# Optimization experiments

Measured on AMD Instinct MI355X. Metric: run time of the kernel, lower is better.

Reference implementation:

```python
import jax, jax.numpy as jnp
import numpy as np

V = 50000

def _spmm(edge_vals, edge_row, edge_col, x):
    # sparse (V,V) @ dense (V,F) via gather + segment_sum
    return jax.ops.segment_sum(edge_vals[:, None] * x[edge_col], edge_row, num_segments=V)

def setup_inputs() -> dict:
    key = jax.random.key(0)
    ks = jax.random.split(key, 6)
    B, Cin, Cout, K, E = 4, 128, 128, 4, 800000
    x = jax.random.normal(ks[0], (B, Cin, V), dtype=jnp.float32)
    edge_row = jax.random.randint(ks[1], (E,), 0, V, dtype=jnp.int32)
    edge_col = jax.random.randint(ks[2], (E,), 0, V, dtype=jnp.int32)
    edge_vals = jax.random.normal(ks[3], (E,), dtype=jnp.float32) * 0.05
    std = np.sqrt(2.0 / (Cin * K)).astype(np.float32)
    weights = jax.random.normal(ks[4], (K, Cin, Cout), dtype=jnp.float32) * std
    biases = jnp.full((Cout,), 0.01, dtype=jnp.float32)
    return {"x": x, "edge_row": edge_row, "edge_col": edge_col,
            "edge_vals": edge_vals, "weights": weights, "biases": biases}

def reference(x, edge_row, edge_col, edge_vals, weights, biases):
    B, Cin, Vv = x.shape
    K = weights.shape[0]
    # (B,Cin,V) -> (V, B*Cin)
    x0 = jnp.transpose(x, (2, 0, 1)).reshape(Vv, B * Cin)
    xs = [x0]
    if K > 1:
        x1 = _spmm(edge_vals, edge_row, edge_col, x0)
        xs.append(x1)
        for _ in range(2, K):
            x2 = 2.0 * _spmm(edge_vals, edge_row, edge_col, x1) - x0
            xs.append(x2)
            x0, x1 = x1, x2
    xk = jnp.stack(xs, 0).reshape(K, Vv, B, Cin)
    # tensordot over (K, Cin): (K,V,B,Cin) x (K,Cin,Cout) -> (V,B,Cout)
    out = jnp.einsum('kvbc,kco->vbo', xk, weights)
    out = out + biases
    # permute (V,B,Cout) -> (B,Cout,V)
    return jnp.transpose(out, (1, 2, 0))
```

## Files before the change

kernel.cpp:

```cpp
#include <hip/hip_runtime.h>

#define V_N   50000
#define B_N   4
#define C_IN  128
#define C_OUT 128
#define E_N   800000
#define F_N   512
#define M_TOT 200000

#define SCAN_BLK  1024
#define SCAN_NB   ((V_N + SCAN_BLK - 1) / SCAN_BLK)

typedef unsigned short ushort_t;
typedef __attribute__((ext_vector_type(8))) short short8;
typedef __attribute__((ext_vector_type(4))) float f32x4;

__device__ __forceinline__ float bf_lo(unsigned u) { return __uint_as_float(u << 16); }
__device__ __forceinline__ float bf_hi(unsigned u) { return __uint_as_float(u & 0xFFFF0000u); }
__device__ __forceinline__ ushort_t f2bf(float f) {
    unsigned u = __float_as_uint(f);
    u += 0x7FFFu + ((u >> 16) & 1u);
    return (ushort_t)(u >> 16);
}

__global__ __launch_bounds__(256) void k_transpose_in(const float* __restrict__ x,
                                                      ushort_t* __restrict__ x0) {
    __shared__ float tile[32][33];
    int vb = blockIdx.x * 32;
    int fb = blockIdx.y * 32;
    int tx = threadIdx.x, ty = threadIdx.y;
#pragma unroll
    for (int i = 0; i < 32; i += 8) {
        int f = fb + ty + i, v = vb + tx;
        float val = 0.f;
        if (v < V_N) val = x[(size_t)f * V_N + v];
        tile[ty + i][tx] = val;
    }
    __syncthreads();
#pragma unroll
    for (int i = 0; i < 32; i += 8) {
        int v = vb + ty + i, f = fb + tx;
        if (v < V_N) x0[(size_t)v * F_N + f] = f2bf(tile[tx][ty + i]);
    }
}

__global__ __launch_bounds__(256) void k_hist(const int* __restrict__ row,
                                              int* __restrict__ counts) {
    int e = blockIdx.x * blockDim.x + threadIdx.x;
    if (e < E_N) atomicAdd(&counts[row[e]], 1);
}

__global__ __launch_bounds__(256) void k_scan_blk(const int* __restrict__ counts,
                                                  int* __restrict__ row_ptr,
                                                  int* __restrict__ blk_sums) {
    __shared__ int s[256];
    int t = threadIdx.x;
    int base = blockIdx.x * SCAN_BLK + t * 4;
    int c0 = (base + 0 < V_N) ? counts[base + 0] : 0;
    int c1 = (base + 1 < V_N) ? counts[base + 1] : 0;
    int c2 = (base + 2 < V_N) ? counts[base + 2] : 0;
    int c3 = (base + 3 < V_N) ? counts[base + 3] : 0;
    int p1 = c0, p2 = c0 + c1, p3 = c0 + c1 + c2, tot = p3 + c3;
    s[t] = tot;
    __syncthreads();
#pragma unroll
    for (int off = 1; off < 256; off <<= 1) {
        int v = (t >= off) ? s[t - off] : 0;
        __syncthreads();
        s[t] += v;
        __syncthreads();
    }
    int excl = (t == 0) ? 0 : s[t - 1];
    if (base + 0 < V_N) row_ptr[base + 0] = excl;
    if (base + 1 < V_N) row_ptr[base + 1] = excl + p1;
    if (base + 2 < V_N) row_ptr[base + 2] = excl + p2;
    if (base + 3 < V_N) row_ptr[base + 3] = excl + p3;
    if (t == 255) blk_sums[blockIdx.x] = s[255];
}

__global__ __launch_bounds__(64) void k_scan_top(const int* __restrict__ blk_sums,
                                                 int* __restrict__ blk_off) {
    int t = threadIdx.x;
    int v = (t < SCAN_NB) ? blk_sums[t] : 0;
#pragma unroll
    for (int off = 1; off < 64; off <<= 1) {
        int u = __shfl_up(v, off);
        if (t >= off) v += u;
    }
    blk_off[t] = v;
}

__global__ __launch_bounds__(256) void k_scan_add(const int* __restrict__ blk_off,
                                                  int* __restrict__ row_ptr,
                                                  int* __restrict__ next) {
    int b = blockIdx.x, t = threadIdx.x;
    int off = (b == 0) ? 0 : blk_off[b - 1];
    int base = b * SCAN_BLK + t * 4;
#pragma unroll
    for (int i = 0; i < 4; i++) {
        int idx = base + i;
        if (idx < V_N) {
            int rv = row_ptr[idx] + off;
            row_ptr[idx] = rv;
            next[idx]    = rv;
        }
    }
    if (b == 0 && t == 0) row_ptr[V_N] = blk_off[SCAN_NB - 1];
}

__global__ __launch_bounds__(256) void k_scatter(const int* __restrict__ row,
                                                 const int* __restrict__ col,
                                                 const float* __restrict__ vals,
                                                 int* __restrict__ next,
                                                 int2* __restrict__ edges) {
    int e = blockIdx.x * blockDim.x + threadIdx.x;
    if (e < E_N) {
        int r = row[e];
        int pos = atomicAdd(&next[r], 1);
        edges[pos] = make_int2(col[e], __float_as_int(vals[e]));
    }
}

__global__ __launch_bounds__(256) void k_wprep(const float* __restrict__ W,
                                               ushort_t* __restrict__ Wt) {
    int i = blockIdx.x * 256 + threadIdx.x;
    int k = i >> 14, c = (i >> 7) & 127, o = i & 127;
    Wt[((size_t)k * 128 + o) * 128 + c] = f2bf(W[i]);
}

__global__ __launch_bounds__(256) void k_spmm_bf16(const int* __restrict__ row_ptr,
                                                   const int2* __restrict__ edges,
                                                   const ushort_t* __restrict__ src,
                                                   const ushort_t* __restrict__ prev,
                                                   ushort_t* __restrict__ dst,
                                                   float alpha, float beta,
                                                   int has_prev) {
    int lane = threadIdx.x & 63;
    int g = blockIdx.x * 4 + (threadIdx.x >> 6);
    int r = g >> 1;
    int h = g & 1;
    int e0 = row_ptr[r], e1 = row_ptr[r + 1];
    float a0 = 0.f, a1 = 0.f, a2 = 0.f, a3 = 0.f;
    const ushort_t* sp = src + h * 256 + lane * 4;

    int e = e0;
    for (; e + 4 <= e1; e += 4) {
        int2 E0 = edges[e], E1 = edges[e + 1], E2 = edges[e + 2], E3 = edges[e + 3];
        uint2 g0 = *(const uint2*)(sp + (size_t)E0.x * F_N);
        uint2 g1 = *(const uint2*)(sp + (size_t)E1.x * F_N);
        uint2 g2 = *(const uint2*)(sp + (size_t)E2.x * F_N);
        uint2 g3 = *(const uint2*)(sp + (size_t)E3.x * F_N);
        float w0 = __int_as_float(E0.y), w1 = __int_as_float(E1.y);
        float w2 = __int_as_float(E2.y), w3 = __int_as_float(E3.y);
        a0 += w0 * bf_lo(g0.x); a1 += w0 * bf_hi(g0.x);
        a2 += w0 * bf_lo(g0.y); a3 += w0 * bf_hi(g0.y);
        a0 += w1 * bf_lo(g1.x); a1 += w1 * bf_hi(g1.x);
        a2 += w1 * bf_lo(g1.y); a3 += w1 * bf_hi(g1.y);
        a0 += w2 * bf_lo(g2.x); a1 += w2 * bf_hi(g2.x);
        a2 += w2 * bf_lo(g2.y); a3 += w2 * bf_hi(g2.y);
        a0 += w3 * bf_lo(g3.x); a1 += w3 * bf_hi(g3.x);
        a2 += w3 * bf_lo(g3.y); a3 += w3 * bf_hi(g3.y);
    }
    for (; e < e1; e++) {
        int2 E = edges[e];
        uint2 gv = *(const uint2*)(sp + (size_t)E.x * F_N);
        float w = __int_as_float(E.y);
        a0 += w * bf_lo(gv.x); a1 += w * bf_hi(gv.x);
        a2 += w * bf_lo(gv.y); a3 += w * bf_hi(gv.y);
    }

    size_t off = (size_t)r * F_N + h * 256 + lane * 4;
    if (has_prev) {
        uint2 pv = *(const uint2*)(prev + off);
        a0 = alpha * a0 + beta * bf_lo(pv.x);
        a1 = alpha * a1 + beta * bf_hi(pv.x);
        a2 = alpha * a2 + beta * bf_lo(pv.y);
        a3 = alpha * a3 + beta * bf_hi(pv.y);
    } else {
        a0 *= alpha; a1 *= alpha; a2 *= alpha; a3 *= alpha;
    }
    ushort_t res[4] = {f2bf(a0), f2bf(a1), f2bf(a2), f2bf(a3)};
    *(uint2*)(dst + off) = *(const uint2*)res;
}

__global__ __launch_bounds__(256, 2) void k_gemm_mfma(
        const ushort_t* __restrict__ X0, const ushort_t* __restrict__ X1,
        const ushort_t* __restrict__ X2, const ushort_t* __restrict__ X3,
        const ushort_t* __restrict__ Wt, const float* __restrict__ bias,
        float* __restrict__ out) {
    __shared__ ushort_t As[128][40];
    __shared__ ushort_t Bs[128][40];
    __shared__ float    Cs[64][133];

    int tid  = threadIdx.x;
    int lane = tid & 63;
    int wave = tid >> 6;
    int wm = wave >> 1, wn = wave & 1;
    int quad = lane >> 4, l15 = lane & 15;
    int m_blk = blockIdx.x * 128;

    f32x4 acc[4][4];
#pragma unroll
    for (int fi = 0; fi < 4; fi++)
#pragma unroll
        for (int fj = 0; fj < 4; fj++) {
            acc[fi][fj][0] = 0.f; acc[fi][fj][1] = 0.f;
            acc[fi][fj][2] = 0.f; acc[fi][fj][3] = 0.f;
        }

    const ushort_t* Xb[4] = {X0, X1, X2, X3};

    for (int kb = 0; kb < 4; kb++) {
        const ushort_t* A = Xb[kb];
        const ushort_t* W = Wt + (size_t)kb * (128 * 128);
        for (int kk = 0; kk < 128; kk += 32) {
            __syncthreads();
#pragma unroll
            for (int i = 0; i < 2; i++) {
                int id = tid + i * 256;
                int rr = id >> 2, p = id & 3;
                int gm = m_blk + rr; if (gm >= M_TOT) gm = M_TOT - 1;
                *(uint4*)&As[rr][p * 8] = *(const uint4*)&A[(size_t)gm * 128 + kk + p * 8];
                *(uint4*)&Bs[rr][p * 8] = *(const uint4*)&W[(size_t)rr * 128 + kk + p * 8];
            }
            __syncthreads();
            short8 a[4], b[4];
#pragma unroll
            for (int f = 0; f < 4; f++) {
                a[f] = *(const short8*)&As[wm * 64 + f * 16 + l15][quad * 8];
                b[f] = *(const short8*)&Bs[wn * 64 + f * 16 + l15][quad * 8];
            }
#pragma unroll
            for (int fi = 0; fi < 4; fi++)
#pragma unroll
                for (int fj = 0; fj < 4; fj++)
                    acc[fi][fj] = __builtin_amdgcn_mfma_f32_16x16x32_bf16(
                        a[fi], b[fj], acc[fi][fj], 0, 0, 0);
        }
    }

    int v_blk = m_blk >> 2;
    for (int h = 0; h < 2; h++) {
        __syncthreads();
        if (wm == h) {
#pragma unroll
            for (int fi = 0; fi < 4; fi++)
#pragma unroll
                for (int fj = 0; fj < 4; fj++) {
                    int ml = fi * 16 + quad * 4;
                    int n  = wn * 64 + fj * 16 + l15;
#pragma unroll
                    for (int reg = 0; reg < 4; reg++)
                        Cs[ml + reg][n] = acc[fi][fj][reg];
                }
        }
        __syncthreads();
#pragma unroll
        for (int i = 0; i < 8; i++) {
            int idx = tid + i * 256;
            int v4  = idx & 3;
            int o   = (idx >> 2) & 127;
            int b   = idx >> 9;
            int vl  = v4 * 4;
            float bv = bias[o];
            float r0 = Cs[(vl + 0) * 4 + b][o] + bv;
            float r1 = Cs[(vl + 1) * 4 + b][o] + bv;
            float r2 = Cs[(vl + 2) * 4 + b][o] + bv;
            float r3 = Cs[(vl + 3) * 4 + b][o] + bv;
            int v0 = v_blk + h * 16 + vl;
            float* op = out + ((size_t)b * C_OUT + o) * V_N + v0;
            if (v0 + 3 < V_N) {
                *(float4*)op = make_float4(r0, r1, r2, r3);
            } else {
                if (v0     < V_N) op[0] = r0;
                if (v0 + 1 < V_N) op[1] = r1;
                if (v0 + 2 < V_N) op[2] = r2;
                if (v0 + 3 < V_N) op[3] = r3;
            }
        }
    }
}

extern "C" void kernel_launch(void* const* d_in, const int* in_sizes, int n_in,
                              void* d_out, int out_size, void* d_ws, size_t ws_size,
                              hipStream_t stream) {
    const float* x        = (const float*)d_in[0];
    const int*   edge_row = (const int*)  d_in[1];
    const int*   edge_col = (const int*)  d_in[2];
    const float* edge_val = (const float*)d_in[3];
    const float* weights  = (const float*)d_in[4];
    const float* biases   = (const float*)d_in[5];
    float* out = (float*)d_out;

    const size_t XSZ = (size_t)V_N * F_N;
    ushort_t* x0 = (ushort_t*)d_ws;
    ushort_t* x1 = x0 + XSZ;
    ushort_t* x2 = x1 + XSZ;
    ushort_t* x3 = x2 + XSZ;
    ushort_t* Wt = x3 + XSZ;
    int* iw      = (int*)(Wt + 4 * 128 * 128);
    int* row_ptr = iw;
    int* counts  = iw + 50016;
    int* nxt     = iw + 100032;
    int* blk_sums= iw + 150048;
    int* blk_off = iw + 150112;
    int2* edges  = (int2*)(iw + 150176);

    dim3 tb(32, 8);
    dim3 tgrid((V_N + 31) / 32, F_N / 32);

    k_transpose_in<<<tgrid, tb, 0, stream>>>(x, x0);

    hipMemsetAsync(counts, 0, V_N * sizeof(int), stream);
    k_hist<<<(E_N + 255) / 256, 256, 0, stream>>>(edge_row, counts);
    k_scan_blk<<<SCAN_NB, 256, 0, stream>>>(counts, row_ptr, blk_sums);
    k_scan_top<<<1, 64, 0, stream>>>(blk_sums, blk_off);
    k_scan_add<<<SCAN_NB, 256, 0, stream>>>(blk_off, row_ptr, nxt);
    k_scatter<<<(E_N + 255) / 256, 256, 0, stream>>>(edge_row, edge_col, edge_val,
                                                     nxt, edges);

    k_wprep<<<256, 256, 0, stream>>>(weights, Wt);

    k_spmm_bf16<<<V_N * 2 / 4, 256, 0, stream>>>(row_ptr, edges, x0, x0, x1,
                                                 1.f, 0.f, 0);
    k_spmm_bf16<<<V_N * 2 / 4, 256, 0, stream>>>(row_ptr, edges, x1, x0, x2,
                                                 2.f, -1.f, 1);
    k_spmm_bf16<<<V_N * 2 / 4, 256, 0, stream>>>(row_ptr, edges, x2, x1, x3,
                                                 2.f, -1.f, 1);

    k_gemm_mfma<<<(M_TOT + 127) / 128, 256, 0, stream>>>(x0, x1, x2, x3, Wt,
                                                         biases, out);
}
```

Baseline: 724.6 us.

## Store features in 32-column chunk-major layout and split SpMM by chunk

The intermediate feature matrices now use a chunked layout: 16 chunks of 32 bf16 columns, each stored contiguously across all vertices. The SpMM launches one grid slice per chunk, so each chunk's working set (about 3.2 MB) can stay in cache while random gathers hit it. Each wave reads four edges at once, with 16 lanes per edge, and combines the partial sums with shuffles. Gathers shrink to 64-byte rows and edge lists are re-read 16 times, so edge traffic rises. The GEMM and transpose indexing were adapted to the new layout.

```diff
diff --git a/kernel.cpp b/kernel.cpp
--- a/kernel.cpp
+++ b/kernel.cpp
@@ -8,6 +8,8 @@
 #define F_N   512
 #define M_TOT 200000
 
+#define NCHUNK 16
+
 #define SCAN_BLK  1024
 #define SCAN_NB   ((V_N + SCAN_BLK - 1) / SCAN_BLK)
 
@@ -40,7 +42,8 @@
 #pragma unroll
     for (int i = 0; i < 32; i += 8) {
         int v = vb + ty + i, f = fb + tx;
-        if (v < V_N) x0[(size_t)v * F_N + f] = f2bf(tile[tx][ty + i]);
+        if (v < V_N)
+            x0[(((size_t)(f >> 5) * V_N + v) << 5) + (f & 31)] = f2bf(tile[tx][ty + i]);
     }
 }
 
@@ -128,59 +131,68 @@
     Wt[((size_t)k * 128 + o) * 128 + c] = f2bf(W[i]);
 }
 
-__global__ __launch_bounds__(256) void k_spmm_bf16(const int* __restrict__ row_ptr,
-                                                   const int2* __restrict__ edges,
-                                                   const ushort_t* __restrict__ src,
-                                                   const ushort_t* __restrict__ prev,
-                                                   ushort_t* __restrict__ dst,
-                                                   float alpha, float beta,
-                                                   int has_prev) {
+__global__ __launch_bounds__(256) void k_spmm_chunk(const int* __restrict__ row_ptr,
+                                                    const int2* __restrict__ edges,
+                                                    const ushort_t* __restrict__ src,
+                                                    const ushort_t* __restrict__ prev,
+                                                    ushort_t* __restrict__ dst,
+                                                    float alpha, float beta,
+                                                    int has_prev) {
     int lane = threadIdx.x & 63;
-    int g = blockIdx.x * 4 + (threadIdx.x >> 6);
-    int r = g >> 1;
-    int h = g & 1;
+    int sub  = lane >> 4;
+    int d    = lane & 15;
+    int r = __builtin_amdgcn_readfirstlane(blockIdx.x * 4 + (threadIdx.x >> 6));
+    int chunk = blockIdx.y;
+    const ushort_t* sc = src + ((size_t)chunk * V_N << 5) + d * 2;
     int e0 = row_ptr[r], e1 = row_ptr[r + 1];
-    float a0 = 0.f, a1 = 0.f, a2 = 0.f, a3 = 0.f;
-    const ushort_t* sp = src + h * 256 + lane * 4;
+    float aL = 0.f, aH = 0.f;
 
     int e = e0;
-    for (; e + 4 <= e1; e += 4) {
-        int2 E0 = edges[e], E1 = edges[e + 1], E2 = edges[e + 2], E3 = edges[e + 3];
-        uint2 g0 = *(const uint2*)(sp + (size_t)E0.x * F_N);
-        uint2 g1 = *(const uint2*)(sp + (size_t)E1.x * F_N);
-        uint2 g2 = *(const uint2*)(sp + (size_t)E2.x * F_N);
-        uint2 g3 = *(const uint2*)(sp + (size_t)E3.x * F_N);
-        float w0 = __int_as_float(E0.y), w1 = __int_as_float(E1.y);
-        float w2 = __int_as_float(E2.y), w3 = __int_as_float(E3.y);
-        a0 += w0 * bf_lo(g0.x); a1 += w0 * bf_hi(g0.x);
-        a2 += w0 * bf_lo(g0.y); a3 += w0 * bf_hi(g0.y);
-        a0 += w1 * bf_lo(g1.x); a1 += w1 * bf_hi(g1.x);
-        a2 += w1 * bf_lo(g1.y); a3 += w1 * bf_hi(g1.y);
-        a0 += w2 * bf_lo(g2.x); a1 += w2 * bf_hi(g2.x);
-        a2 += w2 * bf_lo(g2.y); a3 += w2 * bf_hi(g2.y);
-        a0 += w3 * bf_lo(g3.x); a1 += w3 * bf_hi(g3.x);
-        a2 += w3 * bf_lo(g3.y); a3 += w3 * bf_hi(g3.y);
-    }
-    for (; e < e1; e++) {
-        int2 E = edges[e];
-        uint2 gv = *(const uint2*)(sp + (size_t)E.x * F_N);
-        float w = __int_as_float(E.y);
-        a0 += w * bf_lo(gv.x); a1 += w * bf_hi(gv.x);
-        a2 += w * bf_lo(gv.y); a3 += w * bf_hi(gv.y);
-    }
-
-    size_t off = (size_t)r * F_N + h * 256 + lane * 4;
-    if (has_prev) {
-        uint2 pv = *(const uint2*)(prev + off);
-        a0 = alpha * a0 + beta * bf_lo(pv.x);
-        a1 = alpha * a1 + beta * bf_hi(pv.x);
-        a2 = alpha * a2 + beta * bf_lo(pv.y);
-        a3 = alpha * a3 + beta * bf_hi(pv.y);
-    } else {
-        a0 *= alpha; a1 *= alpha; a2 *= alpha; a3 *= alpha;
-    }
-    ushort_t res[4] = {f2bf(a0), f2bf(a1), f2bf(a2), f2bf(a3)};
-    *(uint2*)(dst + off) = *(const uint2*)res;
+    for (; e + 16 <= e1; e += 16) {
+        unsigned long long v0 = __builtin_nontemporal_load((const unsigned long long*)(edges + e + 0  + sub));
+        unsigned long long v1 = __builtin_nontemporal_load((const unsigned long long*)(edges + e + 4  + sub));
+        unsigned long long v2 = __builtin_nontemporal_load((const unsigned long long*)(edges + e + 8  + sub));
+        unsigned long long v3 = __builtin_nontemporal_load((const unsigned long long*)(edges + e + 12 + sub));
+        unsigned g0 = *(const unsigned*)(sc + ((size_t)(unsigned)(v0 & 0xffffffffu) << 5));
+        unsigned g1 = *(const unsigned*)(sc + ((size_t)(unsigned)(v1 & 0xffffffffu) << 5));
+        unsigned g2 = *(const unsigned*)(sc + ((size_t)(unsigned)(v2 & 0xffffffffu) << 5));
+        unsigned g3 = *(const unsigned*)(sc + ((size_t)(unsigned)(v3 & 0xffffffffu) << 5));
+        float w0 = __uint_as_float((unsigned)(v0 >> 32));
+        float w1 = __uint_as_float((unsigned)(v1 >> 32));
+        float w2 = __uint_as_float((unsigned)(v2 >> 32));
+        float w3 = __uint_as_float((unsigned)(v3 >> 32));
+        aL += w0 * bf_lo(g0); aH += w0 * bf_hi(g0);
+        aL += w1 * bf_lo(g1); aH += w1 * bf_hi(g1);
+        aL += w2 * bf_lo(g2); aH += w2 * bf_hi(g2);
+        aL += w3 * bf_lo(g3); aH += w3 * bf_hi(g3);
+    }
+    for (; e < e1; e += 4) {
+        int eg = e + sub;
+        float wv = 0.f; unsigned gv = 0;
+        if (eg < e1) {
+            unsigned long long ev = __builtin_nontemporal_load((const unsigned long long*)(edges + eg));
+            gv = *(const unsigned*)(sc + ((size_t)(unsigned)(ev & 0xffffffffu) << 5));
+            wv = __uint_as_float((unsigned)(ev >> 32));
+        }
+        aL += wv * bf_lo(gv); aH += wv * bf_hi(gv);
+    }
+
+    aL += __shfl_xor(aL, 16); aL += __shfl_xor(aL, 32);
+    aH += __shfl_xor(aH, 16); aH += __shfl_xor(aH, 32);
+
+    if (sub == 0) {
+        size_t off = ((size_t)chunk * V_N << 5) + ((size_t)r << 5) + d * 2;
+        float rl, rh;
+        if (has_prev) {
+            unsigned pv = __builtin_nontemporal_load((const unsigned*)(prev + off));
+            rl = alpha * aL + beta * bf_lo(pv);
+            rh = alpha * aH + beta * bf_hi(pv);
+        } else {
+            rl = alpha * aL; rh = alpha * aH;
+        }
+        ushort_t res[2] = { f2bf(rl), f2bf(rh) };
+        __builtin_nontemporal_store(*(const unsigned*)res, (unsigned*)(dst + off));
+    }
 }
 
 __global__ __launch_bounds__(256, 2) void k_gemm_mfma(
@@ -220,7 +232,9 @@
                 int id = tid + i * 256;
                 int rr = id >> 2, p = id & 3;
                 int gm = m_blk + rr; if (gm >= M_TOT) gm = M_TOT - 1;
-                *(uint4*)&As[rr][p * 8] = *(const uint4*)&A[(size_t)gm * 128 + kk + p * 8];
+                int v = gm >> 2, bb = gm & 3;
+                *(uint4*)&As[rr][p * 8] =
+                    *(const uint4*)&A[(((size_t)(bb * 4 + (kk >> 5)) * V_N + v) << 5) + p * 8];
                 *(uint4*)&Bs[rr][p * 8] = *(const uint4*)&W[(size_t)rr * 128 + kk + p * 8];
             }
             __syncthreads();
@@ -321,12 +335,13 @@
 
     k_wprep<<<256, 256, 0, stream>>>(weights, Wt);
 
-    k_spmm_bf16<<<V_N * 2 / 4, 256, 0, stream>>>(row_ptr, edges, x0, x0, x1,
-                                                 1.f, 0.f, 0);
-    k_spmm_bf16<<<V_N * 2 / 4, 256, 0, stream>>>(row_ptr, edges, x1, x0, x2,
-                                                 2.f, -1.f, 1);
-    k_spmm_bf16<<<V_N * 2 / 4, 256, 0, stream>>>(row_ptr, edges, x2, x1, x3,
-                                                 2.f, -1.f, 1);
+    dim3 sgrid(V_N / 4, NCHUNK);
+    k_spmm_chunk<<<sgrid, 256, 0, stream>>>(row_ptr, edges, x0, x0, x1,
+                                            1.f, 0.f, 0);
+    k_spmm_chunk<<<sgrid, 256, 0, stream>>>(row_ptr, edges, x1, x0, x2,
+                                            2.f, -1.f, 1);
+    k_spmm_chunk<<<sgrid, 256, 0, stream>>>(row_ptr, edges, x2, x1, x3,
+                                            2.f, -1.f, 1);
 
     k_gemm_mfma<<<(M_TOT + 127) / 128, 256, 0, stream>>>(x0, x1, x2, x3, Wt,
                                                          biases, out);
```

New measurement: 1.548 ms. 114% more time.

## Sort edges within each CSR row by column bucket for gather locality

Applied to the files above, without the earlier changes.

Replaces the per-row counting sort with a two-key counting sort over (row, column>>11) bins, 32 buckets per row. Within each row, edges are now grouped by column range, so the SpMM gathers of source rows touch memory in a more ordered way. The scan now runs over 1.6M bins instead of 50K counters, which adds a larger memset, more scan traffic and an extra mid-level scan kernel.

```diff
diff --git a/kernel.cpp b/kernel.cpp
--- a/kernel.cpp
+++ b/kernel.cpp
@@ -8,8 +8,10 @@
 #define F_N   512
 #define M_TOT 200000
 
-#define SCAN_BLK  1024
-#define SCAN_NB   ((V_N + SCAN_BLK - 1) / SCAN_BLK)
+#define NBKT     32
+#define NBIN     (V_N * NBKT)
+#define BIN_NB   ((NBIN + 1023) / 1024)
+#define NBIN_PAD (BIN_NB * 1024)
 
 typedef unsigned short ushort_t;
 typedef __attribute__((ext_vector_type(8))) short short8;
@@ -44,22 +46,20 @@
     }
 }
 
-__global__ __launch_bounds__(256) void k_hist(const int* __restrict__ row,
-                                              int* __restrict__ counts) {
+__global__ __launch_bounds__(256) void k_hist2(const int* __restrict__ row,
+                                               const int* __restrict__ col,
+                                               int* __restrict__ bins) {
     int e = blockIdx.x * blockDim.x + threadIdx.x;
-    if (e < E_N) atomicAdd(&counts[row[e]], 1);
-}
-
-__global__ __launch_bounds__(256) void k_scan_blk(const int* __restrict__ counts,
-                                                  int* __restrict__ row_ptr,
-                                                  int* __restrict__ blk_sums) {
+    if (e < E_N) atomicAdd(&bins[(row[e] << 5) | (col[e] >> 11)], 1);
+}
+
+__global__ __launch_bounds__(256) void k_bscan_blk(int* __restrict__ bins,
+                                                   int* __restrict__ blk_sums) {
     __shared__ int s[256];
     int t = threadIdx.x;
-    int base = blockIdx.x * SCAN_BLK + t * 4;
-    int c0 = (base + 0 < V_N) ? counts[base + 0] : 0;
-    int c1 = (base + 1 < V_N) ? counts[base + 1] : 0;
-    int c2 = (base + 2 < V_N) ? counts[base + 2] : 0;
-    int c3 = (base + 3 < V_N) ? counts[base + 3] : 0;
+    int base = blockIdx.x * 1024 + t * 4;
+    int c0 = bins[base + 0], c1 = bins[base + 1];
+    int c2 = bins[base + 2], c3 = bins[base + 3];
     int p1 = c0, p2 = c0 + c1, p3 = c0 + c1 + c2, tot = p3 + c3;
     s[t] = tot;
     __syncthreads();
@@ -71,53 +71,59 @@
         __syncthreads();
     }
     int excl = (t == 0) ? 0 : s[t - 1];
-    if (base + 0 < V_N) row_ptr[base + 0] = excl;
-    if (base + 1 < V_N) row_ptr[base + 1] = excl + p1;
-    if (base + 2 < V_N) row_ptr[base + 2] = excl + p2;
-    if (base + 3 < V_N) row_ptr[base + 3] = excl + p3;
+    bins[base + 0] = excl;
+    bins[base + 1] = excl + p1;
+    bins[base + 2] = excl + p2;
+    bins[base + 3] = excl + p3;
     if (t == 255) blk_sums[blockIdx.x] = s[255];
 }
 
-__global__ __launch_bounds__(64) void k_scan_top(const int* __restrict__ blk_sums,
-                                                 int* __restrict__ blk_off) {
+__global__ __launch_bounds__(1024) void k_bscan_mid(const int* __restrict__ blk_sums,
+                                                    int* __restrict__ blk_off) {
+    __shared__ int s[1024];
     int t = threadIdx.x;
-    int v = (t < SCAN_NB) ? blk_sums[t] : 0;
-#pragma unroll
-    for (int off = 1; off < 64; off <<= 1) {
-        int u = __shfl_up(v, off);
-        if (t >= off) v += u;
-    }
-    blk_off[t] = v;
-}
-
-__global__ __launch_bounds__(256) void k_scan_add(const int* __restrict__ blk_off,
-                                                  int* __restrict__ row_ptr,
-                                                  int* __restrict__ next) {
+    int i0 = t * 2, i1 = t * 2 + 1;
+    int a = (i0 < BIN_NB) ? blk_sums[i0] : 0;
+    int b = (i1 < BIN_NB) ? blk_sums[i1] : 0;
+    s[t] = a + b;
+    __syncthreads();
+    for (int off = 1; off < 1024; off <<= 1) {
+        int v = (t >= off) ? s[t - off] : 0;
+        __syncthreads();
+        s[t] += v;
+        __syncthreads();
+    }
+    int excl = (t == 0) ? 0 : s[t - 1];
+    if (i0 < BIN_NB) blk_off[i0] = excl;
+    if (i1 < BIN_NB) blk_off[i1] = excl + a;
+}
+
+__global__ __launch_bounds__(256) void k_bscan_add(const int* __restrict__ blk_off,
+                                                   int* __restrict__ bins,
+                                                   int* __restrict__ row_ptr) {
     int b = blockIdx.x, t = threadIdx.x;
-    int off = (b == 0) ? 0 : blk_off[b - 1];
-    int base = b * SCAN_BLK + t * 4;
+    int off = blk_off[b];
+    int base = b * 1024 + t * 4;
 #pragma unroll
     for (int i = 0; i < 4; i++) {
         int idx = base + i;
-        if (idx < V_N) {
-            int rv = row_ptr[idx] + off;
-            row_ptr[idx] = rv;
-            next[idx]    = rv;
-        }
-    }
-    if (b == 0 && t == 0) row_ptr[V_N] = blk_off[SCAN_NB - 1];
-}
-
-__global__ __launch_bounds__(256) void k_scatter(const int* __restrict__ row,
-                                                 const int* __restrict__ col,
-                                                 const float* __restrict__ vals,
-                                                 int* __restrict__ next,
-                                                 int2* __restrict__ edges) {
+        int rv = bins[idx] + off;
+        bins[idx] = rv;
+        if ((idx & 31) == 0 && (idx >> 5) < V_N) row_ptr[idx >> 5] = rv;
+    }
+    if (b == 0 && t == 0) row_ptr[V_N] = E_N;
+}
+
+__global__ __launch_bounds__(256) void k_scatter2(const int* __restrict__ row,
+                                                  const int* __restrict__ col,
+                                                  const float* __restrict__ vals,
+                                                  int* __restrict__ bins,
+                                                  int2* __restrict__ edges) {
     int e = blockIdx.x * blockDim.x + threadIdx.x;
     if (e < E_N) {
-        int r = row[e];
-        int pos = atomicAdd(&next[r], 1);
-        edges[pos] = make_int2(col[e], __float_as_int(vals[e]));
+        int c = col[e];
+        int pos = atomicAdd(&bins[(row[e] << 5) | (c >> 11)], 1);
+        edges[pos] = make_int2(c, __float_as_int(vals[e]));
     }
 }
 
@@ -300,24 +306,23 @@
     ushort_t* Wt = x3 + XSZ;
     int* iw      = (int*)(Wt + 4 * 128 * 128);
     int* row_ptr = iw;
-    int* counts  = iw + 50016;
-    int* nxt     = iw + 100032;
-    int* blk_sums= iw + 150048;
-    int* blk_off = iw + 150112;
-    int2* edges  = (int2*)(iw + 150176);
+    int* bins    = iw + 50016;
+    int* blk_sums= bins + NBIN_PAD;
+    int* blk_off = blk_sums + 2048;
+    int2* edges  = (int2*)(blk_off + 2048);
 
     dim3 tb(32, 8);
     dim3 tgrid((V_N + 31) / 32, F_N / 32);
 
     k_transpose_in<<<tgrid, tb, 0, stream>>>(x, x0);
 
-    hipMemsetAsync(counts, 0, V_N * sizeof(int), stream);
-    k_hist<<<(E_N + 255) / 256, 256, 0, stream>>>(edge_row, counts);
-    k_scan_blk<<<SCAN_NB, 256, 0, stream>>>(counts, row_ptr, blk_sums);
-    k_scan_top<<<1, 64, 0, stream>>>(blk_sums, blk_off);
-    k_scan_add<<<SCAN_NB, 256, 0, stream>>>(blk_off, row_ptr, nxt);
-    k_scatter<<<(E_N + 255) / 256, 256, 0, stream>>>(edge_row, edge_col, edge_val,
-                                                     nxt, edges);
+    hipMemsetAsync(bins, 0, NBIN_PAD * sizeof(int), stream);
+    k_hist2<<<(E_N + 255) / 256, 256, 0, stream>>>(edge_row, edge_col, bins);
+    k_bscan_blk<<<BIN_NB, 256, 0, stream>>>(bins, blk_sums);
+    k_bscan_mid<<<1, 1024, 0, stream>>>(blk_sums, blk_off);
+    k_bscan_add<<<BIN_NB, 256, 0, stream>>>(blk_off, bins, row_ptr);
+    k_scatter2<<<(E_N + 255) / 256, 256, 0, stream>>>(edge_row, edge_col, edge_val,
+                                                      bins, edges);
 
     k_wprep<<<256, 256, 0, stream>>>(weights, Wt);
 
```

Result: no change. 733.8 us (+1.3%).

## Split SpMM feature dimension into four column-quarter blocks per row group

Applied to the files above, without the earlier changes.

Each SpMM wave now handles one quarter (128 bf16 features) of a row, with 2 features per lane instead of 4. Blocks are arranged so that consecutive blockIdx values cover the four quarters of the same 4-row group, and the grid doubles. This is meant to increase parallelism and to concentrate gathers on narrower column slices for better cache locality. In exchange, each edge (row_ptr, edges) is read twice as often and each gather is a smaller 4-byte load.

```diff
diff --git a/kernel.cpp b/kernel.cpp
--- a/kernel.cpp
+++ b/kernel.cpp
@@ -136,51 +136,45 @@
                                                    float alpha, float beta,
                                                    int has_prev) {
     int lane = threadIdx.x & 63;
-    int g = blockIdx.x * 4 + (threadIdx.x >> 6);
-    int r = g >> 1;
-    int h = g & 1;
+    int wid  = threadIdx.x >> 6;
+    int q    = blockIdx.x & 3;
+    int r    = (blockIdx.x >> 2) * 4 + wid;
     int e0 = row_ptr[r], e1 = row_ptr[r + 1];
-    float a0 = 0.f, a1 = 0.f, a2 = 0.f, a3 = 0.f;
-    const ushort_t* sp = src + h * 256 + lane * 4;
+    float aL = 0.f, aH = 0.f;
+    const ushort_t* sp = src + q * 128 + lane * 2;
 
     int e = e0;
     for (; e + 4 <= e1; e += 4) {
         int2 E0 = edges[e], E1 = edges[e + 1], E2 = edges[e + 2], E3 = edges[e + 3];
-        uint2 g0 = *(const uint2*)(sp + (size_t)E0.x * F_N);
-        uint2 g1 = *(const uint2*)(sp + (size_t)E1.x * F_N);
-        uint2 g2 = *(const uint2*)(sp + (size_t)E2.x * F_N);
-        uint2 g3 = *(const uint2*)(sp + (size_t)E3.x * F_N);
+        unsigned g0 = *(const unsigned*)(sp + (size_t)E0.x * F_N);
+        unsigned g1 = *(const unsigned*)(sp + (size_t)E1.x * F_N);
+        unsigned g2 = *(const unsigned*)(sp + (size_t)E2.x * F_N);
+        unsigned g3 = *(const unsigned*)(sp + (size_t)E3.x * F_N);
         float w0 = __int_as_float(E0.y), w1 = __int_as_float(E1.y);
         float w2 = __int_as_float(E2.y), w3 = __int_as_float(E3.y);
-        a0 += w0 * bf_lo(g0.x); a1 += w0 * bf_hi(g0.x);
-        a2 += w0 * bf_lo(g0.y); a3 += w0 * bf_hi(g0.y);
-        a0 += w1 * bf_lo(g1.x); a1 += w1 * bf_hi(g1.x);
-        a2 += w1 * bf_lo(g1.y); a3 += w1 * bf_hi(g1.y);
-        a0 += w2 * bf_lo(g2.x); a1 += w2 * bf_hi(g2.x);
-        a2 += w2 * bf_lo(g2.y); a3 += w2 * bf_hi(g2.y);
-        a0 += w3 * bf_lo(g3.x); a1 += w3 * bf_hi(g3.x);
-        a2 += w3 * bf_lo(g3.y); a3 += w3 * bf_hi(g3.y);
+        aL += w0 * bf_lo(g0); aH += w0 * bf_hi(g0);
+        aL += w1 * bf_lo(g1); aH += w1 * bf_hi(g1);
+        aL += w2 * bf_lo(g2); aH += w2 * bf_hi(g2);
+        aL += w3 * bf_lo(g3); aH += w3 * bf_hi(g3);
     }
     for (; e < e1; e++) {
         int2 E = edges[e];
-        uint2 gv = *(const uint2*)(sp + (size_t)E.x * F_N);
-        float w = __int_as_float(E.y);
-        a0 += w * bf_lo(gv.x); a1 += w * bf_hi(gv.x);
-        a2 += w * bf_lo(gv.y); a3 += w * bf_hi(gv.y);
-    }
-
-    size_t off = (size_t)r * F_N + h * 256 + lane * 4;
+        unsigned gv = *(const unsigned*)(sp + (size_t)E.x * F_N);
+        float wv = __int_as_float(E.y);
+        aL += wv * bf_lo(gv); aH += wv * bf_hi(gv);
+    }
+
+    size_t off = (size_t)r * F_N + q * 128 + lane * 2;
+    float rl, rh;
     if (has_prev) {
-        uint2 pv = *(const uint2*)(prev + off);
-        a0 = alpha * a0 + beta * bf_lo(pv.x);
-        a1 = alpha * a1 + beta * bf_hi(pv.x);
-        a2 = alpha * a2 + beta * bf_lo(pv.y);
-        a3 = alpha * a3 + beta * bf_hi(pv.y);
+        unsigned pv = *(const unsigned*)(prev + off);
+        rl = alpha * aL + beta * bf_lo(pv);
+        rh = alpha * aH + beta * bf_hi(pv);
     } else {
-        a0 *= alpha; a1 *= alpha; a2 *= alpha; a3 *= alpha;
-    }
-    ushort_t res[4] = {f2bf(a0), f2bf(a1), f2bf(a2), f2bf(a3)};
-    *(uint2*)(dst + off) = *(const uint2*)res;
+        rl = alpha * aL; rh = alpha * aH;
+    }
+    ushort_t res[2] = {f2bf(rl), f2bf(rh)};
+    *(unsigned*)(dst + off) = *(const unsigned*)res;
 }
 
 __global__ __launch_bounds__(256, 2) void k_gemm_mfma(
@@ -321,12 +315,12 @@
 
     k_wprep<<<256, 256, 0, stream>>>(weights, Wt);
 
-    k_spmm_bf16<<<V_N * 2 / 4, 256, 0, stream>>>(row_ptr, edges, x0, x0, x1,
-                                                 1.f, 0.f, 0);
-    k_spmm_bf16<<<V_N * 2 / 4, 256, 0, stream>>>(row_ptr, edges, x1, x0, x2,
-                                                 2.f, -1.f, 1);
-    k_spmm_bf16<<<V_N * 2 / 4, 256, 0, stream>>>(row_ptr, edges, x2, x1, x3,
-                                                 2.f, -1.f, 1);
+    k_spmm_bf16<<<(V_N / 4) * 4, 256, 0, stream>>>(row_ptr, edges, x0, x0, x1,
+                                                   1.f, 0.f, 0);
+    k_spmm_bf16<<<(V_N / 4) * 4, 256, 0, stream>>>(row_ptr, edges, x1, x0, x2,
+                                                   2.f, -1.f, 1);
+    k_spmm_bf16<<<(V_N / 4) * 4, 256, 0, stream>>>(row_ptr, edges, x2, x1, x3,
+                                                   2.f, -1.f, 1);
 
     k_gemm_mfma<<<(M_TOT + 127) / 128, 256, 0, stream>>>(x0, x1, x2, x3, Wt,
                                                          biases, out);
```

Result: slower. 780.7 us (+7.7%).
